# Performance work log

Hardware: AMD Instinct MI355X
Metric: run time of the kernel (lower is better)

## Reference

```python
import jax, jax.numpy as jnp
import numpy as np

NUM_HEADS = 16


def setup_inputs() -> dict:
    key = jax.random.key(0)
    ks = jax.random.split(key, 9)
    B, S, D = 2, 2048, 1024
    scale = 1.0 / np.sqrt(D)
    return {
        "hidden_states": jax.random.normal(ks[0], (B, S, D), dtype=jnp.float32),
        "Wq": jax.random.normal(ks[1], (D, D), dtype=jnp.float32) * scale,
        "bq": jnp.zeros((D,), dtype=jnp.float32),
        "Wk": jax.random.normal(ks[2], (D, D), dtype=jnp.float32) * scale,
        "bk": jnp.zeros((D,), dtype=jnp.float32),
        "Wv": jax.random.normal(ks[3], (D, D), dtype=jnp.float32) * scale,
        "bv": jnp.zeros((D,), dtype=jnp.float32),
        "Wo": jax.random.normal(ks[4], (D, D), dtype=jnp.float32) * scale,
        "bo": jnp.zeros((D,), dtype=jnp.float32),
    }


def reference(hidden_states, Wq, bq, Wk, bk, Wv, bv, Wo, bo):
    B, S, D = hidden_states.shape
    H = NUM_HEADS
    hd = D // H
    # q/k/v projections (torch Linear uses x @ W.T + b)
    q = hidden_states @ Wq.T + bq
    k = hidden_states @ Wk.T + bk
    v = hidden_states @ Wv.T + bv
    # split heads: b s (h d) -> b h s d
    q = q.reshape(B, S, H, hd)
    k = k.reshape(B, S, H, hd)
    v = v.reshape(B, S, H, hd)
    # scaled dot-product attention (non-causal, no mask)
    scale = 1.0 / jnp.sqrt(jnp.asarray(hd, dtype=q.dtype))
    scores = jnp.einsum("bqhd,bkhd->bhqk", q, k) * scale
    probs = jax.nn.softmax(scores, axis=-1)
    attn = jnp.einsum("bhqk,bkhd->bqhd", probs, v)
    # merge heads and output projection
    attn = attn.reshape(B, S, D)
    return attn @ Wo.T + bo
```

## Files before the change

### kernel.cpp

```cpp
#include <hip/hip_runtime.h>

typedef short bf16x8 __attribute__((ext_vector_type(8)));
typedef float f32x4 __attribute__((ext_vector_type(4)));
typedef float float4v __attribute__((ext_vector_type(4)));
typedef unsigned short u16x8 __attribute__((ext_vector_type(8)));
typedef unsigned short u16x4 __attribute__((ext_vector_type(4)));

#define GLL16(g, l_) __builtin_amdgcn_global_load_lds( \
    (const __attribute__((address_space(1))) unsigned int*)(g), \
    (__attribute__((address_space(3))) unsigned int*)(l_), 16, 0, 0)

__device__ __forceinline__ unsigned short f2bf(float x) {
  unsigned u = __float_as_uint(x);
  u += 0x7fff + ((u >> 16) & 1);
  return (unsigned short)(u >> 16);
}

__device__ __forceinline__ unsigned cvtpk_bf16(float a, float b) {
  unsigned r;
  asm("v_cvt_pk_bf16_f32 %0, %1, %2" : "=v"(r) : "v"(a), "v"(b));
  return r;
}

__global__ __launch_bounds__(256) void cast_all_kernel(
    const float* __restrict__ X, const float* __restrict__ Wq,
    const float* __restrict__ Wk, const float* __restrict__ Wv,
    const float* __restrict__ Wo,
    unsigned short* __restrict__ Xb, unsigned short* __restrict__ Wb) {
  int bx = blockIdx.x;
  const float* src; unsigned short* dst; int rel;
  if (bx < 2048) { src = X; dst = Xb; rel = bx; }
  else {
    int wi = (bx - 2048) >> 9; rel = (bx - 2048) & 511;
    src = (wi == 0) ? Wq : (wi == 1) ? Wk : (wi == 2) ? Wv : Wo;
    dst = Wb + ((size_t)wi << 20);
  }
  size_t o = (size_t)rel * 2048 + (size_t)threadIdx.x * 8;
  const float4v* s4 = (const float4v*)(src + o);
  float4v v0 = s4[0], v1 = s4[1];
  u16x8 r;
  r[0]=f2bf(v0[0]); r[1]=f2bf(v0[1]); r[2]=f2bf(v0[2]); r[3]=f2bf(v0[3]);
  r[4]=f2bf(v1[0]); r[5]=f2bf(v1[1]); r[6]=f2bf(v1[2]); r[7]=f2bf(v1[3]);
  *(u16x8*)(dst + o) = r;
}

__global__ __launch_bounds__(512, 1) void qkv_gemm256_kernel(
    const unsigned short* __restrict__ Xb, const unsigned short* __restrict__ Wb,
    const float* __restrict__ bq, const float* __restrict__ bk, const float* __restrict__ bv,
    unsigned short* __restrict__ Q, unsigned short* __restrict__ Kd,
    unsigned short* __restrict__ Vt, float qscale) {
  __shared__ __align__(16) unsigned short lds[2][2][256 * 64];
  const int bx0 = blockIdx.x;
  const int bx = (bx0 & 7) * 24 + (bx0 >> 3);
  const int mb = bx / 12, nb = bx % 12;
  const int t = threadIdx.x, l = t & 63;
  const int wm = (t >> 6) >> 2, wn = (t >> 6) & 3;
  const int l15 = l & 15, lhi = l >> 4, sw7 = l15 & 7;

  const unsigned short* Ag = Xb + (size_t)(mb * 256) * 1024;
  const unsigned short* Bg = Wb + (size_t)(nb * 256) * 1024;

  const int slc = (t & 7) ^ ((t >> 3) & 7);
#define STAGE256(kt_, ba_, bb_)                                                  \
  {                                                                              \
    _Pragma("unroll")                                                            \
    for (int i_ = 0; i_ < 4; ++i_) {                                             \
      const int srow = (t >> 3) + i_ * 64;                                       \
      GLL16(Ag + (size_t)srow * 1024 + (kt_) + slc * 8, (ba_) + (srow * 8 + (t & 7)) * 8); \
      GLL16(Bg + (size_t)srow * 1024 + (kt_) + slc * 8, (bb_) + (srow * 8 + (t & 7)) * 8); \
    }                                                                            \
  }
#define RD256(base_, rowbase_) \
  (*(const bf16x8*)((const char*)(base_) + ((rowbase_) + l15) * 128 + ((KS256 * 4 + lhi) ^ sw7) * 16))

  f32x4 acc[8][4];
#pragma unroll
  for (int mi = 0; mi < 8; ++mi)
#pragma unroll
    for (int ni = 0; ni < 4; ++ni)
#pragma unroll
      for (int r0 = 0; r0 < 4; ++r0) acc[mi][ni][r0] = 0.f;

  STAGE256(0, &lds[0][0][0], &lds[0][1][0]);
  asm volatile("s_waitcnt vmcnt(0)" ::: "memory");
  __builtin_amdgcn_s_barrier();

  int cur = 0;
  for (int kt = 0; kt < 1024; kt += 64) {
    const unsigned short* bA = &lds[cur][0][0];
    const unsigned short* bB = &lds[cur][1][0];
    if (kt + 64 < 1024) STAGE256(kt + 64, &lds[cur ^ 1][0][0], &lds[cur ^ 1][1][0]);

    bf16x8 af[4][2], b0[2][2], b1[2][2];
#pragma unroll
    for (int ks = 0; ks < 2; ++ks) {
      const int KS256 = ks;
#pragma unroll
      for (int mi = 0; mi < 4; ++mi) af[mi][ks] = RD256(bA, wm * 128 + mi * 16);
#pragma unroll
      for (int ni = 0; ni < 2; ++ni) b0[ni][ks] = RD256(bB, wn * 64 + ni * 16);
    }
    __builtin_amdgcn_s_setprio(1);
#pragma unroll
    for (int mi = 0; mi < 4; ++mi)
#pragma unroll
      for (int ni = 0; ni < 2; ++ni)
#pragma unroll
        for (int ks = 0; ks < 2; ++ks)
          acc[mi][ni] = __builtin_amdgcn_mfma_f32_16x16x32_bf16(af[mi][ks], b0[ni][ks], acc[mi][ni], 0, 0, 0);
    __builtin_amdgcn_s_setprio(0);
    __builtin_amdgcn_s_barrier();

#pragma unroll
    for (int ks = 0; ks < 2; ++ks) {
      const int KS256 = ks;
#pragma unroll
      for (int ni = 0; ni < 2; ++ni) b1[ni][ks] = RD256(bB, wn * 64 + (ni + 2) * 16);
    }
    __builtin_amdgcn_s_setprio(1);
#pragma unroll
    for (int mi = 0; mi < 4; ++mi)
#pragma unroll
      for (int ni = 0; ni < 2; ++ni)
#pragma unroll
        for (int ks = 0; ks < 2; ++ks)
          acc[mi][ni + 2] = __builtin_amdgcn_mfma_f32_16x16x32_bf16(af[mi][ks], b1[ni][ks], acc[mi][ni + 2], 0, 0, 0);
    __builtin_amdgcn_s_setprio(0);
    __builtin_amdgcn_s_barrier();

#pragma unroll
    for (int ks = 0; ks < 2; ++ks) {
      const int KS256 = ks;
#pragma unroll
      for (int mi = 0; mi < 4; ++mi) af[mi][ks] = RD256(bA, wm * 128 + (mi + 4) * 16);
    }
    __builtin_amdgcn_s_setprio(1);
#pragma unroll
    for (int mi = 0; mi < 4; ++mi)
#pragma unroll
      for (int ni = 0; ni < 2; ++ni)
#pragma unroll
        for (int ks = 0; ks < 2; ++ks)
          acc[mi + 4][ni] = __builtin_amdgcn_mfma_f32_16x16x32_bf16(af[mi][ks], b0[ni][ks], acc[mi + 4][ni], 0, 0, 0);
    __builtin_amdgcn_s_setprio(0);
    __builtin_amdgcn_s_barrier();

    __builtin_amdgcn_s_setprio(1);
#pragma unroll
    for (int mi = 0; mi < 4; ++mi)
#pragma unroll
      for (int ni = 0; ni < 2; ++ni)
#pragma unroll
        for (int ks = 0; ks < 2; ++ks)
          acc[mi + 4][ni + 2] = __builtin_amdgcn_mfma_f32_16x16x32_bf16(af[mi][ks], b1[ni][ks], acc[mi + 4][ni + 2], 0, 0, 0);
    __builtin_amdgcn_s_setprio(0);
    asm volatile("s_waitcnt vmcnt(0)" ::: "memory");
    __builtin_amdgcn_s_barrier();
    cur ^= 1;
  }
#undef STAGE256
#undef RD256

  const int kind = nb >> 2;
  const float* bias = (kind == 0) ? bq : (kind == 1) ? bk : bv;
#pragma unroll
  for (int mi = 0; mi < 8; ++mi)
#pragma unroll
    for (int ni = 0; ni < 4; ++ni) {
      int gm0 = mb * 256 + wm * 128 + mi * 16 + lhi * 4;
      int gn = nb * 256 + wn * 64 + ni * 16 + l15;
      int gnk = gn & 1023;
      float bb_ = bias[gnk];
      if (kind == 2) {
        int h = gnk >> 6, d = gnk & 63;
        int batch = gm0 >> 11, s = gm0 & 2047;
        int sl = s & 63;
        int slp = (sl & 32) | ((sl & 12) << 1) | ((sl & 16) >> 2);
        int sp = (s & ~63) | slp;
        u16x4 pk;
#pragma unroll
        for (int r0 = 0; r0 < 4; ++r0) pk[r0] = f2bf(acc[mi][ni][r0] + bb_);
        *(u16x4*)(Vt + ((size_t)(batch * 16 + h) * 64 + d) * 2048 + sp) = pk;
      } else if (kind == 0) {
#pragma unroll
        for (int r0 = 0; r0 < 4; ++r0)
          Q[(size_t)(gm0 + r0) * 1024 + gnk] = f2bf((acc[mi][ni][r0] + bb_) * qscale);
      } else {
#pragma unroll
        for (int r0 = 0; r0 < 4; ++r0)
          Kd[(size_t)(gm0 + r0) * 1024 + gnk] = f2bf(acc[mi][ni][r0] + bb_);
      }
    }
}

__global__ __launch_bounds__(256, 3) void attn_kernel(
    const unsigned short* __restrict__ Q, const unsigned short* __restrict__ Kd,
    const unsigned short* __restrict__ Vt, unsigned short* __restrict__ Ao) {
  __shared__ __align__(16) unsigned short lKV[3][8192];
  const int bx0 = blockIdx.x;
  const int bx = (bx0 & 7) * 64 + (bx0 >> 3);
  const int bh = bx >> 4, qb = bx & 15;
  const int b = bh >> 4, h = bh & 15;
  const int t = threadIdx.x, l = t & 63;
  const int l15 = l & 15, lhi = l >> 4;
  const int q0 = b * 2048 + qb * 128 + (t >> 6) * 32;
  const unsigned short* Qp = Q + (size_t)q0 * 1024 + h * 64;
  const unsigned short* Kp = Kd + (size_t)b * 2048 * 1024 + h * 64;
  const unsigned short* Vp = Vt + (size_t)bh * 64 * 2048;

  bf16x8 qa[2][2];
#pragma unroll
  for (int rf = 0; rf < 2; ++rf)
#pragma unroll
    for (int ks = 0; ks < 2; ++ks)
      qa[rf][ks] = *(const bf16x8*)(Qp + (size_t)(rf * 16 + l15) * 1024 + ks * 32 + lhi * 8);

  f32x4 acc[2][4];
  float lsum[2];
#pragma unroll
  for (int rf = 0; rf < 2; ++rf) {
    lsum[rf] = 0.f;
#pragma unroll
    for (int j = 0; j < 4; ++j)
#pragma unroll
      for (int r0 = 0; r0 < 4; ++r0) acc[rf][j][r0] = 0.f;
  }

#define STAGE_KV(kb_, buf_)                                                   \
  {                                                                           \
    { int j = t;       int row = j >> 3, lch = (j & 7) ^ (row & 7);           \
      GLL16(Kp + (size_t)((kb_) + row) * 1024 + lch * 8, (buf_) + j * 8); }   \
    { int j = t + 256; int row = j >> 3, lch = (j & 7) ^ (row & 7);           \
      GLL16(Kp + (size_t)((kb_) + row) * 1024 + lch * 8, (buf_) + j * 8); }   \
    { int j = t;       int row = j >> 3, lch = (j & 7) ^ (row & 7);           \
      GLL16(Vp + (size_t)row * 2048 + (kb_) + lch * 8, (buf_) + 4096 + j * 8); } \
    { int j = t + 256; int row = j >> 3, lch = (j & 7) ^ (row & 7);           \
      GLL16(Vp + (size_t)row * 2048 + (kb_) + lch * 8, (buf_) + 4096 + j * 8); } \
  }

  unsigned short* L0 = &lKV[0][0];
  STAGE_KV(0, L0);
  STAGE_KV(64, L0 + 8192);

  for (int ti = 0; ti < 32; ++ti) {
    const unsigned short* bK = L0 + (ti % 3) * 8192;
    const unsigned short* bV = bK + 4096;
    if (ti < 31) {
      asm volatile("s_waitcnt vmcnt(4)" ::: "memory");
    } else {
      asm volatile("s_waitcnt vmcnt(0)" ::: "memory");
    }
    __builtin_amdgcn_s_barrier();
    if (ti < 30) {
      unsigned short* nbuf = L0 + ((ti + 2) % 3) * 8192;
      STAGE_KV((ti + 2) * 64, nbuf);
    }

    f32x4 st[2][4];
#pragma unroll
    for (int rf = 0; rf < 2; ++rf)
#pragma unroll
      for (int cf = 0; cf < 4; ++cf)
#pragma unroll
        for (int r0 = 0; r0 < 4; ++r0) st[rf][cf][r0] = 0.f;
    __builtin_amdgcn_s_setprio(1);
#pragma unroll
    for (int ks = 0; ks < 2; ++ks) {
      bf16x8 kfr[4];
#pragma unroll
      for (int cf = 0; cf < 4; ++cf)
        kfr[cf] = *(const bf16x8*)(bK + (cf * 16 + l15) * 64 + (((ks * 4 + lhi) ^ (l15 & 7)) << 3));
#pragma unroll
      for (int rf = 0; rf < 2; ++rf)
#pragma unroll
        for (int cf = 0; cf < 4; ++cf)
          st[rf][cf] = __builtin_amdgcn_mfma_f32_16x16x32_bf16(kfr[cf], qa[rf][ks], st[rf][cf], 0, 0, 0);
    }
    __builtin_amdgcn_s_setprio(0);

    unsigned pk[2][4][2];
#pragma unroll
    for (int rf = 0; rf < 2; ++rf)
#pragma unroll
      for (int cf = 0; cf < 4; ++cf) {
        float p0 = __builtin_amdgcn_exp2f(st[rf][cf][0]);
        float p1 = __builtin_amdgcn_exp2f(st[rf][cf][1]);
        float p2 = __builtin_amdgcn_exp2f(st[rf][cf][2]);
        float p3 = __builtin_amdgcn_exp2f(st[rf][cf][3]);
        lsum[rf] += (p0 + p1) + (p2 + p3);
        pk[rf][cf][0] = cvtpk_bf16(p0, p1);
        pk[rf][cf][1] = cvtpk_bf16(p2, p3);
      }

    __builtin_amdgcn_s_setprio(1);
#pragma unroll
    for (int ks = 0; ks < 2; ++ks) {
      bf16x8 pa[2];
#pragma unroll
      for (int rf = 0; rf < 2; ++rf) {
        union { unsigned u[4]; bf16x8 v; } pu;
        pu.u[0] = pk[rf][2 * ks][0];     pu.u[1] = pk[rf][2 * ks][1];
        pu.u[2] = pk[rf][2 * ks + 1][0]; pu.u[3] = pk[rf][2 * ks + 1][1];
        pa[rf] = pu.v;
      }
#pragma unroll
      for (int df = 0; df < 4; ++df) {
        bf16x8 vf = *(const bf16x8*)(bV + (df * 16 + l15) * 64 + (((ks * 4 + lhi) ^ (l15 & 7)) << 3));
#pragma unroll
        for (int rf = 0; rf < 2; ++rf)
          acc[rf][df] = __builtin_amdgcn_mfma_f32_16x16x32_bf16(pa[rf], vf, acc[rf][df], 0, 0, 0);
      }
    }
    __builtin_amdgcn_s_setprio(0);
  }
#undef STAGE_KV

#pragma unroll
  for (int rf = 0; rf < 2; ++rf) {
    lsum[rf] += __shfl_xor(lsum[rf], 16);
    lsum[rf] += __shfl_xor(lsum[rf], 32);
  }
  float rn[2][4];
#pragma unroll
  for (int rf = 0; rf < 2; ++rf)
#pragma unroll
    for (int r0 = 0; r0 < 4; ++r0)
      rn[rf][r0] = 1.0f / __shfl(lsum[rf], lhi * 4 + r0);
#pragma unroll
  for (int rf = 0; rf < 2; ++rf)
#pragma unroll
    for (int r0 = 0; r0 < 4; ++r0) {
      int grow = q0 + rf * 16 + lhi * 4 + r0;
#pragma unroll
      for (int df = 0; df < 4; ++df) {
        int gcol = h * 64 + df * 16 + l15;
        Ao[(size_t)grow * 1024 + gcol] = f2bf(acc[rf][df][r0] * rn[rf][r0]);
      }
    }
}

__global__ __launch_bounds__(512) void out_gemm_kernel(
    const unsigned short* __restrict__ Ab, const unsigned short* __restrict__ Wob,
    const float* __restrict__ bo, float* __restrict__ Out) {
  __shared__ __align__(16) unsigned short lA[128 * 64];
  __shared__ __align__(16) unsigned short lB[128 * 64];
  const int bx0 = blockIdx.x;
  const int bx = (bx0 & 7) * 32 + (bx0 >> 3);
  const int mb = bx >> 3, nb = bx & 7;
  const int t = threadIdx.x, l = t & 63, w = t >> 6;
  const int wr = w >> 1, wc = w & 1;
  const int l15 = l & 15, lhi = l >> 4, sw7 = l15 & 7;
  const unsigned short* Ag = Ab + (size_t)(mb * 128) * 1024;
  const unsigned short* Bg = Wob + (size_t)(nb * 128) * 1024;

  f32x4 acc[2][4];
#pragma unroll
  for (int i = 0; i < 2; ++i)
#pragma unroll
    for (int j = 0; j < 4; ++j)
#pragma unroll
      for (int r0 = 0; r0 < 4; ++r0) acc[i][j][r0] = 0.f;

  for (int kt = 0; kt < 1024; kt += 64) {
    {
      int row = t >> 3, lch = (t & 7) ^ (row & 7);
      GLL16(Ag + (size_t)row * 1024 + kt + lch * 8, lA + t * 8);
      GLL16(Bg + (size_t)row * 1024 + kt + lch * 8, lB + t * 8);
      int j2 = t + 512, row2 = j2 >> 3, lch2 = (j2 & 7) ^ (row2 & 7);
      GLL16(Ag + (size_t)row2 * 1024 + kt + lch2 * 8, lA + j2 * 8);
      GLL16(Bg + (size_t)row2 * 1024 + kt + lch2 * 8, lB + j2 * 8);
    }
    asm volatile("s_waitcnt vmcnt(0)" ::: "memory");
    __syncthreads();
#pragma unroll
    for (int ks = 0; ks < 2; ++ks) {
      bf16x8 af[2], bfr[4];
#pragma unroll
      for (int i = 0; i < 2; ++i)
        af[i] = *(const bf16x8*)(lA + (wr * 32 + i * 16 + l15) * 64 + (((ks * 4 + lhi) ^ sw7) << 3));
#pragma unroll
      for (int j = 0; j < 4; ++j)
        bfr[j] = *(const bf16x8*)(lB + (wc * 64 + j * 16 + l15) * 64 + (((ks * 4 + lhi) ^ sw7) << 3));
#pragma unroll
      for (int i = 0; i < 2; ++i)
#pragma unroll
        for (int j = 0; j < 4; ++j)
          acc[i][j] = __builtin_amdgcn_mfma_f32_16x16x32_bf16(af[i], bfr[j], acc[i][j], 0, 0, 0);
    }
    __syncthreads();
  }

#pragma unroll
  for (int i = 0; i < 2; ++i)
#pragma unroll
    for (int j = 0; j < 4; ++j) {
      int gn = nb * 128 + wc * 64 + j * 16 + l15;
      float bb_ = bo[gn];
      int gm0 = mb * 128 + wr * 32 + i * 16 + lhi * 4;
#pragma unroll
      for (int r0 = 0; r0 < 4; ++r0)
        Out[(size_t)(gm0 + r0) * 1024 + gn] = acc[i][j][r0] + bb_;
    }
}

extern "C" void kernel_launch(void* const* d_in, const int* in_sizes, int n_in,
                              void* d_out, int out_size, void* d_ws, size_t ws_size,
                              hipStream_t stream) {
  const float* X  = (const float*)d_in[0];
  const float* Wq = (const float*)d_in[1];
  const float* bq = (const float*)d_in[2];
  const float* Wk = (const float*)d_in[3];
  const float* bk = (const float*)d_in[4];
  const float* Wv = (const float*)d_in[5];
  const float* bv = (const float*)d_in[6];
  const float* Wo = (const float*)d_in[7];
  const float* bo = (const float*)d_in[8];
  char* ws = (char*)d_ws;
  unsigned short* Xb = (unsigned short*)(ws);
  unsigned short* Wb = (unsigned short*)(ws + ((size_t)8  << 20));
  unsigned short* Qb = (unsigned short*)(ws + ((size_t)16 << 20));
  unsigned short* Kb = (unsigned short*)(ws + ((size_t)24 << 20));
  unsigned short* Vt = (unsigned short*)(ws + ((size_t)32 << 20));
  unsigned short* Ab = (unsigned short*)(ws + ((size_t)40 << 20));

  const float qscale = 1.4426950408889634f / 8.0f;

  cast_all_kernel<<<4096, 256, 0, stream>>>(X, Wq, Wk, Wv, Wo, Xb, Wb);
  qkv_gemm256_kernel<<<192, 512, 0, stream>>>(Xb, Wb, bq, bk, bv, Qb, Kb, Vt, qscale);
  attn_kernel<<<512, 256, 0, stream>>>(Qb, Kb, Vt, Ab);
  out_gemm_kernel<<<256, 512, 0, stream>>>(Ab, Wb + ((size_t)3 << 20), bo, (float*)d_out);
}
```

Measured before the change: 105.8 us.

## Retile QKV GEMM to 128x192 blocks and triple-buffer output GEMM

The QKV projection GEMM moves from 192 blocks of 256x256 to 512 blocks of 128x192. That fills more of the 256 CUs, and the launch bounds now allow more blocks per CU. The output GEMM gains a three-stage LDS ring with prefetch two tiles ahead and partial vmcnt waits, where before it loaded and waited synchronously every k step. The cost is less data reuse per block in the QKV GEMM and more LDS use in the output GEMM.

```diff
diff --git a/kernel.cpp b/kernel.cpp
--- a/kernel.cpp
+++ b/kernel.cpp
@@ -44,133 +44,105 @@
   *(u16x8*)(dst + o) = r;
 }
 
-__global__ __launch_bounds__(512, 1) void qkv_gemm256_kernel(
+__global__ __launch_bounds__(512, 4) void qkv_gemm192_kernel(
     const unsigned short* __restrict__ Xb, const unsigned short* __restrict__ Wb,
     const float* __restrict__ bq, const float* __restrict__ bk, const float* __restrict__ bv,
     unsigned short* __restrict__ Q, unsigned short* __restrict__ Kd,
     unsigned short* __restrict__ Vt, float qscale) {
-  __shared__ __align__(16) unsigned short lds[2][2][256 * 64];
+  __shared__ __align__(16) unsigned short lA[2][128 * 64];
+  __shared__ __align__(16) unsigned short lB[2][192 * 64];
   const int bx0 = blockIdx.x;
-  const int bx = (bx0 & 7) * 24 + (bx0 >> 3);
-  const int mb = bx / 12, nb = bx % 12;
-  const int t = threadIdx.x, l = t & 63;
-  const int wm = (t >> 6) >> 2, wn = (t >> 6) & 3;
+  const int bx = (bx0 & 7) * 64 + (bx0 >> 3);
+  const int nb = bx >> 5, mb = bx & 31;
+  const int t = threadIdx.x, l = t & 63, w = t >> 6;
+  const int wm = w >> 2, wn = w & 3;
   const int l15 = l & 15, lhi = l >> 4, sw7 = l15 & 7;
 
-  const unsigned short* Ag = Xb + (size_t)(mb * 256) * 1024;
-  const unsigned short* Bg = Wb + (size_t)(nb * 256) * 1024;
-
-  const int slc = (t & 7) ^ ((t >> 3) & 7);
-#define STAGE256(kt_, ba_, bb_)                                                  \
+  const unsigned short* Ag = Xb + (size_t)(mb * 128) * 1024;
+  const unsigned short* Bg = Wb + (size_t)(nb * 192) * 1024;
+
+#define STAGEQ(kt_, ba_, bb_)                                                    \
   {                                                                              \
-    _Pragma("unroll")                                                            \
-    for (int i_ = 0; i_ < 4; ++i_) {                                             \
-      const int srow = (t >> 3) + i_ * 64;                                       \
-      GLL16(Ag + (size_t)srow * 1024 + (kt_) + slc * 8, (ba_) + (srow * 8 + (t & 7)) * 8); \
-      GLL16(Bg + (size_t)srow * 1024 + (kt_) + slc * 8, (bb_) + (srow * 8 + (t & 7)) * 8); \
-    }                                                                            \
-  }
-#define RD256(base_, rowbase_) \
-  (*(const bf16x8*)((const char*)(base_) + ((rowbase_) + l15) * 128 + ((KS256 * 4 + lhi) ^ sw7) * 16))
-
-  f32x4 acc[8][4];
-#pragma unroll
-  for (int mi = 0; mi < 8; ++mi)
-#pragma unroll
-    for (int ni = 0; ni < 4; ++ni)
+    { int g = t;        int row = g >> 3, lch = (g & 7) ^ (row & 7);             \
+      GLL16(Ag + (size_t)row * 1024 + (kt_) + lch * 8, (ba_) + g * 8); }         \
+    { int g = t + 512;  int row = g >> 3, lch = (g & 7) ^ (row & 7);             \
+      GLL16(Ag + (size_t)row * 1024 + (kt_) + lch * 8, (ba_) + g * 8); }         \
+    { int g = t;        int row = g >> 3, lch = (g & 7) ^ (row & 7);             \
+      GLL16(Bg + (size_t)row * 1024 + (kt_) + lch * 8, (bb_) + g * 8); }         \
+    { int g = t + 512;  int row = g >> 3, lch = (g & 7) ^ (row & 7);             \
+      GLL16(Bg + (size_t)row * 1024 + (kt_) + lch * 8, (bb_) + g * 8); }         \
+    { int g = t + 1024; int row = g >> 3, lch = (g & 7) ^ (row & 7);             \
+      GLL16(Bg + (size_t)row * 1024 + (kt_) + lch * 8, (bb_) + g * 8); }         \
+  }
+#define RDQ(base_, row_) \
+  (*(const bf16x8*)((const char*)(base_) + (size_t)(row_) * 128 + (((ks * 4 + lhi) ^ sw7) << 4)))
+
+  f32x4 acc[4][3];
+#pragma unroll
+  for (int mi = 0; mi < 4; ++mi)
+#pragma unroll
+    for (int ni = 0; ni < 3; ++ni)
 #pragma unroll
       for (int r0 = 0; r0 < 4; ++r0) acc[mi][ni][r0] = 0.f;
 
-  STAGE256(0, &lds[0][0][0], &lds[0][1][0]);
+  STAGEQ(0, &lA[0][0], &lB[0][0]);
   asm volatile("s_waitcnt vmcnt(0)" ::: "memory");
   __builtin_amdgcn_s_barrier();
 
   int cur = 0;
   for (int kt = 0; kt < 1024; kt += 64) {
-    const unsigned short* bA = &lds[cur][0][0];
-    const unsigned short* bB = &lds[cur][1][0];
-    if (kt + 64 < 1024) STAGE256(kt + 64, &lds[cur ^ 1][0][0], &lds[cur ^ 1][1][0]);
-
-    bf16x8 af[4][2], b0[2][2], b1[2][2];
+    const unsigned short* bA = &lA[cur][0];
+    const unsigned short* bB = &lB[cur][0];
+    if (kt + 64 < 1024) STAGEQ(kt + 64, &lA[cur ^ 1][0], &lB[cur ^ 1][0]);
+
+    bf16x8 bfr[3][2], af[2][2];
 #pragma unroll
     for (int ks = 0; ks < 2; ++ks) {
-      const int KS256 = ks;
-#pragma unroll
-      for (int mi = 0; mi < 4; ++mi) af[mi][ks] = RD256(bA, wm * 128 + mi * 16);
-#pragma unroll
-      for (int ni = 0; ni < 2; ++ni) b0[ni][ks] = RD256(bB, wn * 64 + ni * 16);
+#pragma unroll
+      for (int ni = 0; ni < 3; ++ni) bfr[ni][ks] = RDQ(bB, wn * 48 + ni * 16 + l15);
+#pragma unroll
+      for (int mi = 0; mi < 2; ++mi) af[mi][ks] = RDQ(bA, wm * 64 + mi * 16 + l15);
     }
     __builtin_amdgcn_s_setprio(1);
 #pragma unroll
-    for (int mi = 0; mi < 4; ++mi)
-#pragma unroll
-      for (int ni = 0; ni < 2; ++ni)
+    for (int mi = 0; mi < 2; ++mi)
+#pragma unroll
+      for (int ni = 0; ni < 3; ++ni)
 #pragma unroll
         for (int ks = 0; ks < 2; ++ks)
-          acc[mi][ni] = __builtin_amdgcn_mfma_f32_16x16x32_bf16(af[mi][ks], b0[ni][ks], acc[mi][ni], 0, 0, 0);
+          acc[mi][ni] = __builtin_amdgcn_mfma_f32_16x16x32_bf16(af[mi][ks], bfr[ni][ks], acc[mi][ni], 0, 0, 0);
     __builtin_amdgcn_s_setprio(0);
     __builtin_amdgcn_s_barrier();
 
 #pragma unroll
-    for (int ks = 0; ks < 2; ++ks) {
-      const int KS256 = ks;
-#pragma unroll
-      for (int ni = 0; ni < 2; ++ni) b1[ni][ks] = RD256(bB, wn * 64 + (ni + 2) * 16);
-    }
+    for (int ks = 0; ks < 2; ++ks)
+#pragma unroll
+      for (int mi = 0; mi < 2; ++mi) af[mi][ks] = RDQ(bA, wm * 64 + (mi + 2) * 16 + l15);
     __builtin_amdgcn_s_setprio(1);
 #pragma unroll
-    for (int mi = 0; mi < 4; ++mi)
-#pragma unroll
-      for (int ni = 0; ni < 2; ++ni)
+    for (int mi = 0; mi < 2; ++mi)
+#pragma unroll
+      for (int ni = 0; ni < 3; ++ni)
 #pragma unroll
         for (int ks = 0; ks < 2; ++ks)
-          acc[mi][ni + 2] = __builtin_amdgcn_mfma_f32_16x16x32_bf16(af[mi][ks], b1[ni][ks], acc[mi][ni + 2], 0, 0, 0);
-    __builtin_amdgcn_s_setprio(0);
-    __builtin_amdgcn_s_barrier();
-
-#pragma unroll
-    for (int ks = 0; ks < 2; ++ks) {
-      const int KS256 = ks;
-#pragma unroll
-      for (int mi = 0; mi < 4; ++mi) af[mi][ks] = RD256(bA, wm * 128 + (mi + 4) * 16);
-    }
-    __builtin_amdgcn_s_setprio(1);
-#pragma unroll
-    for (int mi = 0; mi < 4; ++mi)
-#pragma unroll
-      for (int ni = 0; ni < 2; ++ni)
-#pragma unroll
-        for (int ks = 0; ks < 2; ++ks)
-          acc[mi + 4][ni] = __builtin_amdgcn_mfma_f32_16x16x32_bf16(af[mi][ks], b0[ni][ks], acc[mi + 4][ni], 0, 0, 0);
-    __builtin_amdgcn_s_setprio(0);
-    __builtin_amdgcn_s_barrier();
-
-    __builtin_amdgcn_s_setprio(1);
-#pragma unroll
-    for (int mi = 0; mi < 4; ++mi)
-#pragma unroll
-      for (int ni = 0; ni < 2; ++ni)
-#pragma unroll
-        for (int ks = 0; ks < 2; ++ks)
-          acc[mi + 4][ni + 2] = __builtin_amdgcn_mfma_f32_16x16x32_bf16(af[mi][ks], b1[ni][ks], acc[mi + 4][ni + 2], 0, 0, 0);
+          acc[mi + 2][ni] = __builtin_amdgcn_mfma_f32_16x16x32_bf16(af[mi][ks], bfr[ni][ks], acc[mi + 2][ni], 0, 0, 0);
     __builtin_amdgcn_s_setprio(0);
     asm volatile("s_waitcnt vmcnt(0)" ::: "memory");
     __builtin_amdgcn_s_barrier();
     cur ^= 1;
   }
-#undef STAGE256
-#undef RD256
-
-  const int kind = nb >> 2;
-  const float* bias = (kind == 0) ? bq : (kind == 1) ? bk : bv;
-#pragma unroll
-  for (int mi = 0; mi < 8; ++mi)
-#pragma unroll
-    for (int ni = 0; ni < 4; ++ni) {
-      int gm0 = mb * 256 + wm * 128 + mi * 16 + lhi * 4;
-      int gn = nb * 256 + wn * 64 + ni * 16 + l15;
-      int gnk = gn & 1023;
-      float bb_ = bias[gnk];
+#undef STAGEQ
+#undef RDQ
+
+#pragma unroll
+  for (int ni = 0; ni < 3; ++ni) {
+    int gn = nb * 192 + wn * 48 + ni * 16 + l15;
+    int kind = gn >> 10, gnk = gn & 1023;
+    const float* bias = (kind == 0) ? bq : (kind == 1) ? bk : bv;
+    float bb_ = bias[gnk];
+#pragma unroll
+    for (int mi = 0; mi < 4; ++mi) {
+      int gm0 = mb * 128 + wm * 64 + mi * 16 + lhi * 4;
       if (kind == 2) {
         int h = gnk >> 6, d = gnk & 63;
         int batch = gm0 >> 11, s = gm0 & 2047;
@@ -191,6 +163,7 @@
           Kd[(size_t)(gm0 + r0) * 1024 + gnk] = f2bf(acc[mi][ni][r0] + bb_);
       }
     }
+  }
 }
 
 __global__ __launch_bounds__(256, 3) void attn_kernel(
@@ -339,11 +312,11 @@
     }
 }
 
-__global__ __launch_bounds__(512) void out_gemm_kernel(
+__global__ __launch_bounds__(512, 2) void out_gemm_kernel(
     const unsigned short* __restrict__ Ab, const unsigned short* __restrict__ Wob,
     const float* __restrict__ bo, float* __restrict__ Out) {
-  __shared__ __align__(16) unsigned short lA[128 * 64];
-  __shared__ __align__(16) unsigned short lB[128 * 64];
+  __shared__ __align__(16) unsigned short lA[3][128 * 64];
+  __shared__ __align__(16) unsigned short lB[3][128 * 64];
   const int bx0 = blockIdx.x;
   const int bx = (bx0 & 7) * 32 + (bx0 >> 3);
   const int mb = bx >> 3, nb = bx & 7;
@@ -353,6 +326,18 @@
   const unsigned short* Ag = Ab + (size_t)(mb * 128) * 1024;
   const unsigned short* Bg = Wob + (size_t)(nb * 128) * 1024;
 
+#define STAGEO(kt_, ba_, bb_)                                                    \
+  {                                                                              \
+    { int g = t;       int row = g >> 3, lch = (g & 7) ^ (row & 7);              \
+      GLL16(Ag + (size_t)row * 1024 + (kt_) + lch * 8, (ba_) + g * 8); }         \
+    { int g = t + 512; int row = g >> 3, lch = (g & 7) ^ (row & 7);              \
+      GLL16(Ag + (size_t)row * 1024 + (kt_) + lch * 8, (ba_) + g * 8); }         \
+    { int g = t;       int row = g >> 3, lch = (g & 7) ^ (row & 7);              \
+      GLL16(Bg + (size_t)row * 1024 + (kt_) + lch * 8, (bb_) + g * 8); }         \
+    { int g = t + 512; int row = g >> 3, lch = (g & 7) ^ (row & 7);              \
+      GLL16(Bg + (size_t)row * 1024 + (kt_) + lch * 8, (bb_) + g * 8); }         \
+  }
+
   f32x4 acc[2][4];
 #pragma unroll
   for (int i = 0; i < 2; ++i)
@@ -361,34 +346,39 @@
 #pragma unroll
       for (int r0 = 0; r0 < 4; ++r0) acc[i][j][r0] = 0.f;
 
-  for (int kt = 0; kt < 1024; kt += 64) {
-    {
-      int row = t >> 3, lch = (t & 7) ^ (row & 7);
-      GLL16(Ag + (size_t)row * 1024 + kt + lch * 8, lA + t * 8);
-      GLL16(Bg + (size_t)row * 1024 + kt + lch * 8, lB + t * 8);
-      int j2 = t + 512, row2 = j2 >> 3, lch2 = (j2 & 7) ^ (row2 & 7);
-      GLL16(Ag + (size_t)row2 * 1024 + kt + lch2 * 8, lA + j2 * 8);
-      GLL16(Bg + (size_t)row2 * 1024 + kt + lch2 * 8, lB + j2 * 8);
-    }
-    asm volatile("s_waitcnt vmcnt(0)" ::: "memory");
-    __syncthreads();
+  STAGEO(0, &lA[0][0], &lB[0][0]);
+  STAGEO(64, &lA[1][0], &lB[1][0]);
+
+  for (int ti = 0; ti < 16; ++ti) {
+    const unsigned short* bA = &lA[ti % 3][0];
+    const unsigned short* bB = &lB[ti % 3][0];
+    if (ti < 15) {
+      asm volatile("s_waitcnt vmcnt(4)" ::: "memory");
+    } else {
+      asm volatile("s_waitcnt vmcnt(0)" ::: "memory");
+    }
+    __builtin_amdgcn_s_barrier();
+    if (ti < 14) STAGEO((ti + 2) * 64, &lA[(ti + 2) % 3][0], &lB[(ti + 2) % 3][0]);
+
 #pragma unroll
     for (int ks = 0; ks < 2; ++ks) {
       bf16x8 af[2], bfr[4];
 #pragma unroll
       for (int i = 0; i < 2; ++i)
-        af[i] = *(const bf16x8*)(lA + (wr * 32 + i * 16 + l15) * 64 + (((ks * 4 + lhi) ^ sw7) << 3));
+        af[i] = *(const bf16x8*)(bA + (wr * 32 + i * 16 + l15) * 64 + (((ks * 4 + lhi) ^ sw7) << 3));
 #pragma unroll
       for (int j = 0; j < 4; ++j)
-        bfr[j] = *(const bf16x8*)(lB + (wc * 64 + j * 16 + l15) * 64 + (((ks * 4 + lhi) ^ sw7) << 3));
+        bfr[j] = *(const bf16x8*)(bB + (wc * 64 + j * 16 + l15) * 64 + (((ks * 4 + lhi) ^ sw7) << 3));
+      __builtin_amdgcn_s_setprio(1);
 #pragma unroll
       for (int i = 0; i < 2; ++i)
 #pragma unroll
         for (int j = 0; j < 4; ++j)
           acc[i][j] = __builtin_amdgcn_mfma_f32_16x16x32_bf16(af[i], bfr[j], acc[i][j], 0, 0, 0);
-    }
-    __syncthreads();
-  }
+      __builtin_amdgcn_s_setprio(0);
+    }
+  }
+#undef STAGEO
 
 #pragma unroll
   for (int i = 0; i < 2; ++i)
@@ -426,7 +416,7 @@
   const float qscale = 1.4426950408889634f / 8.0f;
 
   cast_all_kernel<<<4096, 256, 0, stream>>>(X, Wq, Wk, Wv, Wo, Xb, Wb);
-  qkv_gemm256_kernel<<<192, 512, 0, stream>>>(Xb, Wb, bq, bk, bv, Qb, Kb, Vt, qscale);
+  qkv_gemm192_kernel<<<512, 512, 0, stream>>>(Xb, Wb, bq, bk, bv, Qb, Kb, Vt, qscale);
   attn_kernel<<<512, 256, 0, stream>>>(Qb, Kb, Vt, Ab);
   out_gemm_kernel<<<256, 512, 0, stream>>>(Ab, Wb + ((size_t)3 << 20), bo, (float*)d_out);
 }
```

New measurement: 99.59 us, median of 2. -5.9%, faster.
